# Kernel optimization log

Measured on AMD Instinct MI355X. Metric: run time of the kernel, lower is better.

The kernel has to match this reference:

```python
import jax, jax.numpy as jnp
import numpy as np

INTRINSIC_DIM = 3  # all linear dims, no periodic dims
EPS = 1e-10


def _cdist(a, b):
    # Euclidean distance via the expanded form; clamp for numerical safety.
    sq = (jnp.sum(a * a, axis=1)[:, None]
          + jnp.sum(b * b, axis=1)[None, :]
          - 2.0 * (a @ b.T))
    return jnp.sqrt(jnp.maximum(sq, 0.0))


def _thin_plate_kernel(r, dim):
    r_safe = jnp.maximum(r, EPS)
    if dim == 2:
        k = r_safe ** 2 * jnp.log(r_safe)
    else:
        k = r_safe ** (dim - 2) * jnp.log(r_safe)
    return jnp.where(r < EPS, jnp.zeros_like(k), k)


def setup_inputs() -> dict:
    key = jax.random.key(0)
    k1, k2, k3, k4 = jax.random.split(key, 4)
    batch, n, d, amb = 16384, 4096, INTRINSIC_DIM, 3
    m = 1 + d  # constant + one linear term per (non-periodic) dim
    u = jax.random.uniform(k1, (batch, d), dtype=jnp.float32)
    control_points = jax.random.uniform(k2, (n, d), dtype=jnp.float32)
    rbf_weights = jax.random.normal(k3, (n, amb), dtype=jnp.float32)
    poly_coeffs = jax.random.normal(k4, (m, amb), dtype=jnp.float32)
    return {"u": u, "control_points": control_points,
            "rbf_weights": rbf_weights, "poly_coeffs": poly_coeffs}


def reference(u, control_points, rbf_weights, poly_coeffs):
    # K_query: (batch, n) TPS kernel on pairwise Euclidean distances
    dists = _cdist(u, control_points)
    K_query = _thin_plate_kernel(dists, dim=INTRINSIC_DIM)
    # Polynomial matrix: [1, x] over all linear dims -> (batch, 1 + d)
    P_query = jnp.concatenate([jnp.ones((u.shape[0], 1), dtype=u.dtype), u], axis=1)
    return K_query @ rbf_weights + P_query @ poly_coeffs
```

## Files before the change

kernel.cpp:

```cpp
#include <hip/hip_runtime.h>


typedef float v2f __attribute__((ext_vector_type(2)));
typedef float v4f __attribute__((ext_vector_type(4)));

#define BLK 256
#define NS 4
#define QPT 4
#define QPB 256
#define JCHUNK 128
#define JW (JCHUNK / NS)

__global__ __launch_bounds__(BLK, 8) void tps_kernel(
    const float* __restrict__ u,
    const float* __restrict__ cp,
    const float* __restrict__ w,
    const float* __restrict__ poly,
    float* __restrict__ out,
    int batch, int n)
{
    __shared__ v4f s_a4[JCHUNK * 2];
    __shared__ v4f s_b4[JCHUNK * 2];
    __shared__ float s_red[NS][QPB * 3];

    const float C = 0.34657359027997264f;

    const int tid = threadIdx.x;
    const int j0 = blockIdx.y * JCHUNK;

    if (tid < JCHUNK) {
        const int g = j0 + tid;
        const float cx = cp[g * 3 + 0], cy = cp[g * 3 + 1], cz = cp[g * 3 + 2];
        const float c2 = fmaf(cx, cx, fmaf(cy, cy, cz * cz));
        const float wx = C * w[g * 3 + 0];
        const float wy = C * w[g * 3 + 1];
        const float wz = C * w[g * 3 + 2];
        s_a4[tid * 2 + 0] = (v4f){-2.f * cx, -2.f * cx, -2.f * cy, -2.f * cy};
        s_a4[tid * 2 + 1] = (v4f){-2.f * cz, -2.f * cz, c2, c2};
        s_b4[tid * 2 + 0] = (v4f){wx, wx, wy, wy};
        s_b4[tid * 2 + 1] = (v4f){wz, wz, 0.f, 0.f};
    }
    __syncthreads();

    const int lane = tid & 63;
    const int wv   = tid >> 6;

    v2f uxv[2], uyv[2], uzv[2], usqv[2];
    v2f axv[2], ayv[2], azv[2];
#pragma unroll
    for (int g = 0; g < 2; ++g) {
        const int qa = blockIdx.x * QPB + (2 * g + 0) * 64 + lane;
        const int qb = blockIdx.x * QPB + (2 * g + 1) * 64 + lane;
        uxv[g] = (v2f){u[qa * 3 + 0], u[qb * 3 + 0]};
        uyv[g] = (v2f){u[qa * 3 + 1], u[qb * 3 + 1]};
        uzv[g] = (v2f){u[qa * 3 + 2], u[qb * 3 + 2]};
        usqv[g] = __builtin_elementwise_fma(uxv[g], uxv[g],
                  __builtin_elementwise_fma(uyv[g], uyv[g], uzv[g] * uzv[g]));
        axv[g] = (v2f){0.f, 0.f};
        ayv[g] = (v2f){0.f, 0.f};
        azv[g] = (v2f){0.f, 0.f};
    }

    if (blockIdx.y == 0 && wv == 0) {
#pragma unroll
        for (int g = 0; g < 2; ++g) {
            axv[g] = poly[0] + uxv[g] * poly[3] + uyv[g] * poly[6] + uzv[g] * poly[9];
            ayv[g] = poly[1] + uxv[g] * poly[4] + uyv[g] * poly[7] + uzv[g] * poly[10];
            azv[g] = poly[2] + uxv[g] * poly[5] + uyv[g] * poly[8] + uzv[g] * poly[11];
        }
    }

    const int jlo = wv * JW;
#pragma unroll 2
    for (int j = jlo; j < jlo + JW; ++j) {
        const v4f A0 = s_a4[j * 2 + 0];
        const v4f A1 = s_a4[j * 2 + 1];
        const v4f B0 = s_b4[j * 2 + 0];
        const v4f B1 = s_b4[j * 2 + 1];
        const v2f m2x = A0.xy, m2y = A0.zw, m2z = A1.xy, c2v = A1.zw;
        const v2f wxv = B0.xy, wyv = B0.zw, wzv = B1.xy;
#pragma unroll
        for (int g = 0; g < 2; ++g) {
            v2f r2 = __builtin_elementwise_fma(m2x, uxv[g],
                     __builtin_elementwise_fma(m2y, uyv[g],
                     __builtin_elementwise_fma(m2z, uzv[g], c2v + usqv[g])));
            r2 = __builtin_elementwise_max(r2, (v2f){1e-30f, 1e-30f});
            const v2f sq = {__builtin_amdgcn_sqrtf(r2.x),
                            __builtin_amdgcn_sqrtf(r2.y)};
            const v2f lg = {__builtin_amdgcn_logf(r2.x),
                            __builtin_amdgcn_logf(r2.y)};
            const v2f kk = sq * lg;
            axv[g] = __builtin_elementwise_fma(kk, wxv, axv[g]);
            ayv[g] = __builtin_elementwise_fma(kk, wyv, ayv[g]);
            azv[g] = __builtin_elementwise_fma(kk, wzv, azv[g]);
        }
    }

#pragma unroll
    for (int g = 0; g < 2; ++g) {
        const int ba = ((2 * g + 0) * 64 + lane) * 3;
        const int bb = ((2 * g + 1) * 64 + lane) * 3;
        s_red[wv][ba + 0] = axv[g].x;  s_red[wv][bb + 0] = axv[g].y;
        s_red[wv][ba + 1] = ayv[g].x;  s_red[wv][bb + 1] = ayv[g].y;
        s_red[wv][ba + 2] = azv[g].x;  s_red[wv][bb + 2] = azv[g].y;
    }
    __syncthreads();

    for (int v = tid; v < QPB * 3; v += BLK) {
        float s = s_red[0][v] + s_red[1][v] + s_red[2][v] + s_red[3][v];
        atomicAdd(&out[(size_t)blockIdx.x * (QPB * 3) + v], s);
    }
}

extern "C" void kernel_launch(void* const* d_in, const int* in_sizes, int n_in,
                              void* d_out, int out_size, void* d_ws, size_t ws_size,
                              hipStream_t stream) {
    const float* u    = (const float*)d_in[0];
    const float* cp   = (const float*)d_in[1];
    const float* w    = (const float*)d_in[2];
    const float* poly = (const float*)d_in[3];
    float* out = (float*)d_out;

    const int batch = in_sizes[0] / 3;
    const int n     = in_sizes[1] / 3;

    hipMemsetAsync(d_out, 0, (size_t)out_size * sizeof(float), stream);

    dim3 block(BLK);
    dim3 grid(batch / QPB, n / JCHUNK);
    tps_kernel<<<grid, block, 0, stream>>>(u, cp, w, poly, out, batch, n);
}
```

Before: 79.29 us.

## Precompute control-point records in a prep kernel and drop shared-memory reduction

Adds a separate prep kernel that packs the control-point terms and scaled weights into a workspace array once, instead of each block rebuilding them in shared memory. The main kernel now gives each wave its own 256 queries (1024 queries per block) over a 32-point j chunk, reading the records directly from global memory as uniform loads. Each thread then does atomic adds of its partial sums straight to the output, with no shared-memory reduction. This removes the shared-memory staging and the block barriers. In exchange it issues many more global atomics (n/32 partials per output) and drops the packed v2f math.

```diff
diff --git a/kernel.cpp b/kernel.cpp
--- a/kernel.cpp
+++ b/kernel.cpp
@@ -1,114 +1,90 @@
 #include <hip/hip_runtime.h>
 
 
-typedef float v2f __attribute__((ext_vector_type(2)));
 typedef float v4f __attribute__((ext_vector_type(4)));
 
 #define BLK 256
-#define NS 4
 #define QPT 4
-#define QPB 256
-#define JCHUNK 128
-#define JW (JCHUNK / NS)
+#define QPW (64 * QPT)
+#define NWV 4
+#define QPB (QPW * NWV)
+#define JBLK 32
+
+__global__ void tps_prep(const float* __restrict__ cp,
+                         const float* __restrict__ w,
+                         float* __restrict__ rec, int n)
+{
+    const float C = 0.34657359027997264f;
+    const int j = blockIdx.x * blockDim.x + threadIdx.x;
+    if (j >= n) return;
+    const float cx = cp[j * 3 + 0], cy = cp[j * 3 + 1], cz = cp[j * 3 + 2];
+    v4f a = {-2.f * cx, -2.f * cy, -2.f * cz,
+             fmaf(cx, cx, fmaf(cy, cy, cz * cz))};
+    v4f b = {C * w[j * 3 + 0], C * w[j * 3 + 1], C * w[j * 3 + 2], 0.f};
+    ((v4f*)rec)[j * 2 + 0] = a;
+    ((v4f*)rec)[j * 2 + 1] = b;
+}
 
 __global__ __launch_bounds__(BLK, 8) void tps_kernel(
     const float* __restrict__ u,
-    const float* __restrict__ cp,
-    const float* __restrict__ w,
+    const float* __restrict__ rec,
     const float* __restrict__ poly,
     float* __restrict__ out,
     int batch, int n)
 {
-    __shared__ v4f s_a4[JCHUNK * 2];
-    __shared__ v4f s_b4[JCHUNK * 2];
-    __shared__ float s_red[NS][QPB * 3];
-
-    const float C = 0.34657359027997264f;
-
-    const int tid = threadIdx.x;
-    const int j0 = blockIdx.y * JCHUNK;
-
-    if (tid < JCHUNK) {
-        const int g = j0 + tid;
-        const float cx = cp[g * 3 + 0], cy = cp[g * 3 + 1], cz = cp[g * 3 + 2];
-        const float c2 = fmaf(cx, cx, fmaf(cy, cy, cz * cz));
-        const float wx = C * w[g * 3 + 0];
-        const float wy = C * w[g * 3 + 1];
-        const float wz = C * w[g * 3 + 2];
-        s_a4[tid * 2 + 0] = (v4f){-2.f * cx, -2.f * cx, -2.f * cy, -2.f * cy};
-        s_a4[tid * 2 + 1] = (v4f){-2.f * cz, -2.f * cz, c2, c2};
-        s_b4[tid * 2 + 0] = (v4f){wx, wx, wy, wy};
-        s_b4[tid * 2 + 1] = (v4f){wz, wz, 0.f, 0.f};
-    }
-    __syncthreads();
-
+    const int tid  = threadIdx.x;
     const int lane = tid & 63;
     const int wv   = tid >> 6;
+    const int q0   = blockIdx.x * QPB + wv * QPW + lane;
 
-    v2f uxv[2], uyv[2], uzv[2], usqv[2];
-    v2f axv[2], ayv[2], azv[2];
+    float ux[QPT], uy[QPT], uz[QPT], usq[QPT];
+    float ax[QPT], ay[QPT], az[QPT];
 #pragma unroll
-    for (int g = 0; g < 2; ++g) {
-        const int qa = blockIdx.x * QPB + (2 * g + 0) * 64 + lane;
-        const int qb = blockIdx.x * QPB + (2 * g + 1) * 64 + lane;
-        uxv[g] = (v2f){u[qa * 3 + 0], u[qb * 3 + 0]};
-        uyv[g] = (v2f){u[qa * 3 + 1], u[qb * 3 + 1]};
-        uzv[g] = (v2f){u[qa * 3 + 2], u[qb * 3 + 2]};
-        usqv[g] = __builtin_elementwise_fma(uxv[g], uxv[g],
-                  __builtin_elementwise_fma(uyv[g], uyv[g], uzv[g] * uzv[g]));
-        axv[g] = (v2f){0.f, 0.f};
-        ayv[g] = (v2f){0.f, 0.f};
-        azv[g] = (v2f){0.f, 0.f};
+    for (int k = 0; k < QPT; ++k) {
+        const int q = q0 + k * 64;
+        ux[k] = u[q * 3 + 0];
+        uy[k] = u[q * 3 + 1];
+        uz[k] = u[q * 3 + 2];
+        usq[k] = fmaf(ux[k], ux[k], fmaf(uy[k], uy[k], uz[k] * uz[k]));
+        ax[k] = 0.f; ay[k] = 0.f; az[k] = 0.f;
     }
 
-    if (blockIdx.y == 0 && wv == 0) {
+    if (blockIdx.y == 0) {
 #pragma unroll
-        for (int g = 0; g < 2; ++g) {
-            axv[g] = poly[0] + uxv[g] * poly[3] + uyv[g] * poly[6] + uzv[g] * poly[9];
-            ayv[g] = poly[1] + uxv[g] * poly[4] + uyv[g] * poly[7] + uzv[g] * poly[10];
-            azv[g] = poly[2] + uxv[g] * poly[5] + uyv[g] * poly[8] + uzv[g] * poly[11];
+        for (int k = 0; k < QPT; ++k) {
+            ax[k] = poly[0] + ux[k] * poly[3] + uy[k] * poly[6] + uz[k] * poly[9];
+            ay[k] = poly[1] + ux[k] * poly[4] + uy[k] * poly[7] + uz[k] * poly[10];
+            az[k] = poly[2] + ux[k] * poly[5] + uy[k] * poly[8] + uz[k] * poly[11];
         }
     }
 
-    const int jlo = wv * JW;
+    const v4f* __restrict__ rec4 = (const v4f*)rec;
+    const int j0 = blockIdx.y * JBLK;
 #pragma unroll 2
-    for (int j = jlo; j < jlo + JW; ++j) {
-        const v4f A0 = s_a4[j * 2 + 0];
-        const v4f A1 = s_a4[j * 2 + 1];
-        const v4f B0 = s_b4[j * 2 + 0];
-        const v4f B1 = s_b4[j * 2 + 1];
-        const v2f m2x = A0.xy, m2y = A0.zw, m2z = A1.xy, c2v = A1.zw;
-        const v2f wxv = B0.xy, wyv = B0.zw, wzv = B1.xy;
+    for (int j = j0; j < j0 + JBLK; ++j) {
+        const v4f A = rec4[j * 2 + 0];
+        const v4f B = rec4[j * 2 + 1];
 #pragma unroll
-        for (int g = 0; g < 2; ++g) {
-            v2f r2 = __builtin_elementwise_fma(m2x, uxv[g],
-                     __builtin_elementwise_fma(m2y, uyv[g],
-                     __builtin_elementwise_fma(m2z, uzv[g], c2v + usqv[g])));
-            r2 = __builtin_elementwise_max(r2, (v2f){1e-30f, 1e-30f});
-            const v2f sq = {__builtin_amdgcn_sqrtf(r2.x),
-                            __builtin_amdgcn_sqrtf(r2.y)};
-            const v2f lg = {__builtin_amdgcn_logf(r2.x),
-                            __builtin_amdgcn_logf(r2.y)};
-            const v2f kk = sq * lg;
-            axv[g] = __builtin_elementwise_fma(kk, wxv, axv[g]);
-            ayv[g] = __builtin_elementwise_fma(kk, wyv, ayv[g]);
-            azv[g] = __builtin_elementwise_fma(kk, wzv, azv[g]);
+        for (int k = 0; k < QPT; ++k) {
+            float r2 = fmaf(A.x, ux[k],
+                       fmaf(A.y, uy[k],
+                       fmaf(A.z, uz[k], A.w + usq[k])));
+            r2 = fmaxf(r2, 1e-30f);
+            const float sq = __builtin_amdgcn_sqrtf(r2);
+            const float lg = __builtin_amdgcn_logf(r2);
+            const float kk = sq * lg;
+            ax[k] = fmaf(kk, B.x, ax[k]);
+            ay[k] = fmaf(kk, B.y, ay[k]);
+            az[k] = fmaf(kk, B.z, az[k]);
         }
     }
 
 #pragma unroll
-    for (int g = 0; g < 2; ++g) {
-        const int ba = ((2 * g + 0) * 64 + lane) * 3;
-        const int bb = ((2 * g + 1) * 64 + lane) * 3;
-        s_red[wv][ba + 0] = axv[g].x;  s_red[wv][bb + 0] = axv[g].y;
-        s_red[wv][ba + 1] = ayv[g].x;  s_red[wv][bb + 1] = ayv[g].y;
-        s_red[wv][ba + 2] = azv[g].x;  s_red[wv][bb + 2] = azv[g].y;
-    }
-    __syncthreads();
-
-    for (int v = tid; v < QPB * 3; v += BLK) {
-        float s = s_red[0][v] + s_red[1][v] + s_red[2][v] + s_red[3][v];
-        atomicAdd(&out[(size_t)blockIdx.x * (QPB * 3) + v], s);
+    for (int k = 0; k < QPT; ++k) {
+        const int q = q0 + k * 64;
+        atomicAdd(&out[q * 3 + 0], ax[k]);
+        atomicAdd(&out[q * 3 + 1], ay[k]);
+        atomicAdd(&out[q * 3 + 2], az[k]);
     }
 }
 
@@ -120,13 +96,16 @@
     const float* w    = (const float*)d_in[2];
     const float* poly = (const float*)d_in[3];
     float* out = (float*)d_out;
+    float* rec = (float*)d_ws;
 
     const int batch = in_sizes[0] / 3;
     const int n     = in_sizes[1] / 3;
 
     hipMemsetAsync(d_out, 0, (size_t)out_size * sizeof(float), stream);
 
+    tps_prep<<<dim3((n + BLK - 1) / BLK), dim3(BLK), 0, stream>>>(cp, w, rec, n);
+
     dim3 block(BLK);
-    dim3 grid(batch / QPB, n / JCHUNK);
-    tps_kernel<<<grid, block, 0, stream>>>(u, cp, w, poly, out, batch, n);
+    dim3 grid(batch / QPB, n / JBLK);
+    tps_kernel<<<grid, block, 0, stream>>>(u, rec, poly, out, batch, n);
 }
```

Measured after the change: 130.1 us. +64.1%, slower.
